# Kernel optimization log

Measured on AMD Instinct MI355X. Metric: run time of the kernel, lower is better.

The kernel has to match this reference:

```python
import jax, jax.numpy as jnp
import numpy as np

EPS = 1e-6

def setup_inputs() -> dict:
    key = jax.random.key(0)
    k1, k2 = jax.random.split(key)
    S, B, H, F = 2048, 4, 2048, 8192
    x = jax.random.normal(k1, (S, B, H), dtype=jnp.float32)
    scale = jnp.ones((H,), dtype=jnp.float32)
    ln_bias = jnp.zeros((H,), dtype=jnp.float32)
    kernel = jax.random.normal(k2, (H, F), dtype=jnp.float32) * 0.02  # ~variance_scaling fan_in
    return {"x": x, "scale": scale, "ln_bias": ln_bias, "kernel": kernel}

def reference(x, scale, ln_bias, kernel):
    # LayerNorm over last (hidden) axis, stats in fp32
    mu = jnp.mean(x, axis=-1, keepdims=True)
    var = jnp.mean(jnp.square(x - mu), axis=-1, keepdims=True)
    y = (x - mu) * jax.lax.rsqrt(var + EPS) * scale + ln_bias  # [S,B,H]
    # Dense: contract hidden axis against kernel [H,F]
    z = jnp.einsum('sbh,hf->sbf', y, kernel)  # [S,B,F]
    # return_layernorm_output=True -> (dense_out, ln_out)
    return (z, y)
```

## Files before the change

kernel.cpp:

```cpp
#include <hip/hip_runtime.h>
#include <stdint.h>


typedef __attribute__((ext_vector_type(8))) short short8;
typedef __attribute__((ext_vector_type(4))) float floatx4;

__device__ __forceinline__ unsigned short f2bf(float f) {
    unsigned u = __builtin_bit_cast(unsigned, f);
    u += 0x7fffu + ((u >> 16) & 1u);
    return (unsigned short)(u >> 16);
}

__global__ __launch_bounds__(256) void ln_kernel(
    const float* __restrict__ x, const float* __restrict__ scale,
    const float* __restrict__ bias, float* __restrict__ y,
    unsigned short* __restrict__ ybf, int H)
{
    const int row = blockIdx.x;
    const float* xr = x + (size_t)row * H;
    const int tid = threadIdx.x;

    float4 v0 = ((const float4*)xr)[tid];
    float4 v1 = ((const float4*)xr)[tid + 256];

    float s  = v0.x + v0.y + v0.z + v0.w + v1.x + v1.y + v1.z + v1.w;
    float ss = v0.x*v0.x + v0.y*v0.y + v0.z*v0.z + v0.w*v0.w
             + v1.x*v1.x + v1.y*v1.y + v1.z*v1.z + v1.w*v1.w;

    #pragma unroll
    for (int off = 32; off > 0; off >>= 1) {
        s  += __shfl_down(s,  off, 64);
        ss += __shfl_down(ss, off, 64);
    }
    __shared__ float rs[4], rq[4];
    if ((tid & 63) == 0) { rs[tid >> 6] = s; rq[tid >> 6] = ss; }
    __syncthreads();
    float ts = rs[0] + rs[1] + rs[2] + rs[3];
    float tq = rq[0] + rq[1] + rq[2] + rq[3];
    float mean = ts / (float)H;
    float var  = tq / (float)H - mean * mean;
    float rstd = rsqrtf(var + 1e-6f);

    float4 sc0 = ((const float4*)scale)[tid];
    float4 sc1 = ((const float4*)scale)[tid + 256];
    float4 b0  = ((const float4*)bias)[tid];
    float4 b1  = ((const float4*)bias)[tid + 256];

    float4 o0, o1;
    o0.x = (v0.x - mean) * rstd * sc0.x + b0.x;
    o0.y = (v0.y - mean) * rstd * sc0.y + b0.y;
    o0.z = (v0.z - mean) * rstd * sc0.z + b0.z;
    o0.w = (v0.w - mean) * rstd * sc0.w + b0.w;
    o1.x = (v1.x - mean) * rstd * sc1.x + b1.x;
    o1.y = (v1.y - mean) * rstd * sc1.y + b1.y;
    o1.z = (v1.z - mean) * rstd * sc1.z + b1.z;
    o1.w = (v1.w - mean) * rstd * sc1.w + b1.w;

    float* yr = y + (size_t)row * H;
    ((float4*)yr)[tid]       = o0;
    ((float4*)yr)[tid + 256] = o1;

    unsigned short* br = ybf + (size_t)row * H;
    uint2 p0, p1;
    p0.x = (unsigned)f2bf(o0.x) | ((unsigned)f2bf(o0.y) << 16);
    p0.y = (unsigned)f2bf(o0.z) | ((unsigned)f2bf(o0.w) << 16);
    p1.x = (unsigned)f2bf(o1.x) | ((unsigned)f2bf(o1.y) << 16);
    p1.y = (unsigned)f2bf(o1.z) | ((unsigned)f2bf(o1.w) << 16);
    ((uint2*)br)[tid]       = p0;
    ((uint2*)br)[tid + 256] = p1;
}

__global__ __launch_bounds__(256) void transpose_cast_kernel(
    const float* __restrict__ W, unsigned short* __restrict__ Bt,
    int K, int F)
{
    __shared__ float tile[64][65];
    const int kBase = blockIdx.y * 64;
    const int fBase = blockIdx.x * 64;
    const int tid = threadIdx.x;

    #pragma unroll
    for (int p = 0; p < 4; ++p) {
        int kl = (tid >> 4) + p * 16;
        int fl = (tid & 15) * 4;
        float4 v = *(const float4*)&W[(size_t)(kBase + kl) * F + fBase + fl];
        tile[kl][fl]     = v.x;
        tile[kl][fl + 1] = v.y;
        tile[kl][fl + 2] = v.z;
        tile[kl][fl + 3] = v.w;
    }
    __syncthreads();

    #pragma unroll
    for (int p = 0; p < 2; ++p) {
        int fl = (tid >> 3) + p * 32;
        int k8 = (tid & 7) * 8;
        unsigned w[4];
        #pragma unroll
        for (int j = 0; j < 4; ++j) {
            unsigned lo = f2bf(tile[k8 + 2*j][fl]);
            unsigned hi = f2bf(tile[k8 + 2*j + 1][fl]);
            w[j] = lo | (hi << 16);
        }
        uint4 out = make_uint4(w[0], w[1], w[2], w[3]);
        *(uint4*)&Bt[(size_t)(fBase + fl) * K + kBase + k8] = out;
    }
}

#define GBM 256
#define GBN 256
#define GBK 64

__device__ __forceinline__ void gload16(const unsigned short* src,
                                        unsigned short* dst) {
    __builtin_amdgcn_global_load_lds(
        (const __attribute__((address_space(1))) unsigned int*)src,
        (__attribute__((address_space(3))) unsigned int*)dst, 16, 0, 0);
}

__device__ __forceinline__ void stage_tile(
    const unsigned short* __restrict__ gA,
    const unsigned short* __restrict__ gB,
    unsigned short* dst, int t, int K, int o0, int d0)
{
    const int kb = t * GBK;
    #pragma unroll
    for (int j = 0; j < 4; ++j)
        gload16(gA + (size_t)(o0 + j * 64 * K + kb), dst + j * 4096 + d0);
    #pragma unroll
    for (int j = 0; j < 4; ++j)
        gload16(gB + (size_t)(o0 + j * 64 * K + kb), dst + 16384 + j * 4096 + d0);
}

template<int MH, int NH, bool LA, bool LB>
__device__ __forceinline__ void quad_phase(
    const unsigned short* bufA, const unsigned short* bufB,
    int rowA, int rowB, int s0, int s1,
    short8 (&a)[4][2], short8 (&b)[2][2], floatx4 (&acc)[8][4])
{
    if (LA) {
        #pragma unroll
        for (int i = 0; i < 4; ++i) {
            const unsigned short* rp = bufA + (MH * 64 + i * 16) * 64 + rowA;
            a[i][0] = *(const short8*)(rp + s0);
            a[i][1] = *(const short8*)(rp + s1);
        }
    }
    if (LB) {
        #pragma unroll
        for (int j = 0; j < 2; ++j) {
            const unsigned short* rp = bufB + ((NH * 2 + j) * 16) * 64 + rowB;
            b[j][0] = *(const short8*)(rp + s0);
            b[j][1] = *(const short8*)(rp + s1);
        }
    }
    __builtin_amdgcn_s_barrier();
    __builtin_amdgcn_s_setprio(1);
    #pragma unroll
    for (int i = 0; i < 4; ++i)
        #pragma unroll
        for (int j = 0; j < 2; ++j) {
            acc[MH*4+i][NH*2+j] = __builtin_amdgcn_mfma_f32_16x16x32_bf16(
                a[i][0], b[j][0], acc[MH*4+i][NH*2+j], 0, 0, 0);
            acc[MH*4+i][NH*2+j] = __builtin_amdgcn_mfma_f32_16x16x32_bf16(
                a[i][1], b[j][1], acc[MH*4+i][NH*2+j], 0, 0, 0);
        }
    __builtin_amdgcn_s_setprio(0);
    __builtin_amdgcn_s_barrier();
}

__global__ __launch_bounds__(512, 2) void gemm_bf16_8w(
    const unsigned short* __restrict__ A,
    const unsigned short* __restrict__ Bt,
    float* __restrict__ C,
    int M, int N, int K)
{
    __shared__ __align__(128) unsigned short lds[2][32768];

    const int tid   = threadIdx.x;
    const int lane  = tid & 63;
    const int wave  = tid >> 6;
    const int waveM = wave >> 2;
    const int waveN = wave & 3;
    const int quad  = lane >> 4;
    const int l16   = lane & 15;
    const int xs    = l16 & 7;
    const int s0    = (quad ^ xs) * 8;
    const int s1    = ((4 | quad) ^ xs) * 8;
    const int rowA  = l16 * 64;
    const int rowB  = ((waveN & 1) * 64 + l16) * 64;

    const int r0 = tid >> 3;
    const int g0 = (tid & 7) ^ (r0 & 7);
    const int o0 = r0 * K + g0 * 8;
    const int d0 = tid * 8;

    const int nwg = gridDim.x;
    const int cpx = nwg >> 3;
    const int bid = blockIdx.x;
    const int wg  = (bid & 7) * cpx + (bid >> 3);
    const int tilesN = N >> 8;
    const int tm = wg / tilesN;
    const int tn = wg % tilesN;

    const unsigned short* gA = A  + (size_t)tm * GBM * K;
    const unsigned short* gB = Bt + (size_t)tn * GBN * K;

    const int NT = K >> 6;

    floatx4 acc[8][4] = {};
    short8 a[4][2], b[2][2];

    unsigned short* bufA0 = &lds[0][0] + waveM * 8192;
    unsigned short* bufB0 = &lds[0][0] + 16384 + (waveN >> 1) * 8192;

    stage_tile(gA, gB, &lds[0][0], 0, K, o0, d0);
    stage_tile(gA, gB, &lds[1][0], 1, K, o0, d0);
    asm volatile("s_waitcnt vmcnt(8)" ::: "memory");
    __builtin_amdgcn_s_barrier();

    for (int t = 0; t < NT; t += 2) {
        quad_phase<0,0,true ,true >(bufA0, bufB0, rowA, rowB, s0, s1, a, b, acc);
        quad_phase<0,1,false,true >(bufA0, bufB0, rowA, rowB, s0, s1, a, b, acc);
        quad_phase<1,1,true ,false>(bufA0, bufB0, rowA, rowB, s0, s1, a, b, acc);
        quad_phase<1,0,false,true >(bufA0, bufB0, rowA, rowB, s0, s1, a, b, acc);
        {
            int ts = (t + 2 < NT) ? (t + 2) : (NT - 1);
            stage_tile(gA, gB, &lds[0][0], ts, K, o0, d0);
            asm volatile("s_waitcnt vmcnt(8)" ::: "memory");
            __builtin_amdgcn_s_barrier();
        }
        quad_phase<0,0,true ,true >(bufA0 + 32768, bufB0 + 32768, rowA, rowB, s0, s1, a, b, acc);
        quad_phase<0,1,false,true >(bufA0 + 32768, bufB0 + 32768, rowA, rowB, s0, s1, a, b, acc);
        quad_phase<1,1,true ,false>(bufA0 + 32768, bufB0 + 32768, rowA, rowB, s0, s1, a, b, acc);
        quad_phase<1,0,false,true >(bufA0 + 32768, bufB0 + 32768, rowA, rowB, s0, s1, a, b, acc);
        {
            int ts = (t + 3 < NT) ? (t + 3) : (NT - 1);
            stage_tile(gA, gB, &lds[1][0], ts, K, o0, d0);
            asm volatile("s_waitcnt vmcnt(8)" ::: "memory");
            __builtin_amdgcn_s_barrier();
        }
    }

    const size_t bm = (size_t)tm * GBM;
    const size_t bn = (size_t)tn * GBN;
    #pragma unroll
    for (int mi = 0; mi < 8; ++mi) {
        #pragma unroll
        for (int ni = 0; ni < 4; ++ni) {
            size_t col = bn + (size_t)waveN * 64 + ni * 16 + l16;
            #pragma unroll
            for (int r = 0; r < 4; ++r) {
                size_t row = bm + (size_t)waveM * 128 + mi * 16 + quad * 4 + r;
                C[row * N + col] = acc[mi][ni][r];
            }
        }
    }
}

extern "C" void kernel_launch(void* const* d_in, const int* in_sizes, int n_in,
                              void* d_out, int out_size, void* d_ws, size_t ws_size,
                              hipStream_t stream) {
    const float* x      = (const float*)d_in[0];
    const float* scale  = (const float*)d_in[1];
    const float* lnbias = (const float*)d_in[2];
    const float* W      = (const float*)d_in[3];

    const int H = in_sizes[1];
    const int M = in_sizes[0] / H;
    const int F = in_sizes[3] / H;

    float* z = (float*)d_out;
    float* y = z + (size_t)M * F;

    unsigned short* Abf = (unsigned short*)d_ws;
    unsigned short* Btb = Abf + (size_t)M * H;

    ln_kernel<<<M, 256, 0, stream>>>(x, scale, lnbias, y, Abf, H);
    transpose_cast_kernel<<<dim3(F / 64, H / 64), 256, 0, stream>>>(W, Btb, H, F);
    gemm_bf16_8w<<<dim3((M / GBM) * (F / GBN)), 512, 0, stream>>>(Abf, Btb, z, M, F, H);
}
```

Baseline: 705.6 us.

## Switch GEMM mainloop to 4-stage BK=32 pipeline with interleaved prefetch

Restructures the bf16 GEMM main loop from a double-buffered BK=64 scheme into a four-stage ring of BK=32 tiles, prefetching three tiles ahead. Each A and B tile load is issued between the LDS fragment reads and the MFMA block, and a new XOR swizzle is used for 32-wide rows. The aim is deeper latency hiding for global-to-LDS loads and fewer LDS reads per MFMA batch. The cost is twice as many barriers per unit of K, and the hand-tuned vmcnt accounting may not match the new load count.

```diff
diff --git a/kernel.cpp b/kernel.cpp
--- a/kernel.cpp
+++ b/kernel.cpp
@@ -109,7 +109,7 @@
 
 #define GBM 256
 #define GBN 256
-#define GBK 64
+#define GBK 32
 
 __device__ __forceinline__ void gload16(const unsigned short* src,
                                         unsigned short* dst) {
@@ -118,55 +118,17 @@
         (__attribute__((address_space(3))) unsigned int*)dst, 16, 0, 0);
 }
 
-__device__ __forceinline__ void stage_tile(
-    const unsigned short* __restrict__ gA,
-    const unsigned short* __restrict__ gB,
-    unsigned short* dst, int t, int K, int o0, int d0)
-{
-    const int kb = t * GBK;
-    #pragma unroll
-    for (int j = 0; j < 4; ++j)
-        gload16(gA + (size_t)(o0 + j * 64 * K + kb), dst + j * 4096 + d0);
-    #pragma unroll
-    for (int j = 0; j < 4; ++j)
-        gload16(gB + (size_t)(o0 + j * 64 * K + kb), dst + 16384 + j * 4096 + d0);
-}
-
-template<int MH, int NH, bool LA, bool LB>
-__device__ __forceinline__ void quad_phase(
-    const unsigned short* bufA, const unsigned short* bufB,
-    int rowA, int rowB, int s0, int s1,
-    short8 (&a)[4][2], short8 (&b)[2][2], floatx4 (&acc)[8][4])
-{
-    if (LA) {
-        #pragma unroll
-        for (int i = 0; i < 4; ++i) {
-            const unsigned short* rp = bufA + (MH * 64 + i * 16) * 64 + rowA;
-            a[i][0] = *(const short8*)(rp + s0);
-            a[i][1] = *(const short8*)(rp + s1);
-        }
-    }
-    if (LB) {
-        #pragma unroll
-        for (int j = 0; j < 2; ++j) {
-            const unsigned short* rp = bufB + ((NH * 2 + j) * 16) * 64 + rowB;
-            b[j][0] = *(const short8*)(rp + s0);
-            b[j][1] = *(const short8*)(rp + s1);
-        }
-    }
-    __builtin_amdgcn_s_barrier();
-    __builtin_amdgcn_s_setprio(1);
-    #pragma unroll
-    for (int i = 0; i < 4; ++i)
-        #pragma unroll
-        for (int j = 0; j < 2; ++j) {
-            acc[MH*4+i][NH*2+j] = __builtin_amdgcn_mfma_f32_16x16x32_bf16(
-                a[i][0], b[j][0], acc[MH*4+i][NH*2+j], 0, 0, 0);
-            acc[MH*4+i][NH*2+j] = __builtin_amdgcn_mfma_f32_16x16x32_bf16(
-                a[i][1], b[j][1], acc[MH*4+i][NH*2+j], 0, 0, 0);
-        }
-    __builtin_amdgcn_s_setprio(0);
-    __builtin_amdgcn_s_barrier();
+__device__ __forceinline__ void stage_op(
+    const unsigned short* __restrict__ g, unsigned short* dst,
+    int t, int K, int tid)
+{
+    #pragma unroll
+    for (int i = 0; i < 2; ++i) {
+        int e = i * 512 + tid;
+        int r = e >> 2;
+        int c = (e & 3) ^ ((r >> 1) & 3);
+        gload16(g + (size_t)r * K + t * GBK + c * 8, dst + e * 8);
+    }
 }
 
 __global__ __launch_bounds__(512, 2) void gemm_bf16_8w(
@@ -175,7 +137,7 @@
     float* __restrict__ C,
     int M, int N, int K)
 {
-    __shared__ __align__(128) unsigned short lds[2][32768];
+    __shared__ __align__(128) unsigned short lds[4][16384];
 
     const int tid   = threadIdx.x;
     const int lane  = tid & 63;
@@ -184,16 +146,9 @@
     const int waveN = wave & 3;
     const int quad  = lane >> 4;
     const int l16   = lane & 15;
-    const int xs    = l16 & 7;
-    const int s0    = (quad ^ xs) * 8;
-    const int s1    = ((4 | quad) ^ xs) * 8;
-    const int rowA  = l16 * 64;
-    const int rowB  = ((waveN & 1) * 64 + l16) * 64;
-
-    const int r0 = tid >> 3;
-    const int g0 = (tid & 7) ^ (r0 & 7);
-    const int o0 = r0 * K + g0 * 8;
-    const int d0 = tid * 8;
+    const int soff  = (quad ^ ((l16 >> 1) & 3)) * 8;
+    const int rowA0 = waveM * 128 + l16;
+    const int rowB0 = waveN * 64 + l16;
 
     const int nwg = gridDim.x;
     const int cpx = nwg >> 3;
@@ -206,37 +161,66 @@
     const unsigned short* gA = A  + (size_t)tm * GBM * K;
     const unsigned short* gB = Bt + (size_t)tn * GBN * K;
 
-    const int NT = K >> 6;
+    const int NT = K >> 5;
 
     floatx4 acc[8][4] = {};
-    short8 a[4][2], b[2][2];
-
-    unsigned short* bufA0 = &lds[0][0] + waveM * 8192;
-    unsigned short* bufB0 = &lds[0][0] + 16384 + (waveN >> 1) * 8192;
-
-    stage_tile(gA, gB, &lds[0][0], 0, K, o0, d0);
-    stage_tile(gA, gB, &lds[1][0], 1, K, o0, d0);
+
+    stage_op(gA, &lds[0][0],    0, K, tid);
+    stage_op(gB, &lds[0][8192], 0, K, tid);
+    stage_op(gA, &lds[1][0],    1, K, tid);
+    stage_op(gB, &lds[1][8192], 1, K, tid);
+    stage_op(gA, &lds[2][0],    2, K, tid);
+    stage_op(gB, &lds[2][8192], 2, K, tid);
     asm volatile("s_waitcnt vmcnt(8)" ::: "memory");
     __builtin_amdgcn_s_barrier();
 
-    for (int t = 0; t < NT; t += 2) {
-        quad_phase<0,0,true ,true >(bufA0, bufB0, rowA, rowB, s0, s1, a, b, acc);
-        quad_phase<0,1,false,true >(bufA0, bufB0, rowA, rowB, s0, s1, a, b, acc);
-        quad_phase<1,1,true ,false>(bufA0, bufB0, rowA, rowB, s0, s1, a, b, acc);
-        quad_phase<1,0,false,true >(bufA0, bufB0, rowA, rowB, s0, s1, a, b, acc);
-        {
-            int ts = (t + 2 < NT) ? (t + 2) : (NT - 1);
-            stage_tile(gA, gB, &lds[0][0], ts, K, o0, d0);
-            asm volatile("s_waitcnt vmcnt(8)" ::: "memory");
-            __builtin_amdgcn_s_barrier();
-        }
-        quad_phase<0,0,true ,true >(bufA0 + 32768, bufB0 + 32768, rowA, rowB, s0, s1, a, b, acc);
-        quad_phase<0,1,false,true >(bufA0 + 32768, bufB0 + 32768, rowA, rowB, s0, s1, a, b, acc);
-        quad_phase<1,1,true ,false>(bufA0 + 32768, bufB0 + 32768, rowA, rowB, s0, s1, a, b, acc);
-        quad_phase<1,0,false,true >(bufA0 + 32768, bufB0 + 32768, rowA, rowB, s0, s1, a, b, acc);
-        {
-            int ts = (t + 3 < NT) ? (t + 3) : (NT - 1);
-            stage_tile(gA, gB, &lds[1][0], ts, K, o0, d0);
+    for (int t = 0; t < NT; t += 4) {
+        #pragma unroll
+        for (int u = 0; u < 4; ++u) {
+            const int tt = t + u;
+            const unsigned short* bufA = &lds[u][0];
+            const unsigned short* bufB = &lds[u][8192];
+            unsigned short* pre = &lds[(u + 3) & 3][0];
+            int ts = tt + 3; if (ts > NT - 1) ts = NT - 1;
+
+            short8 a[4], b[4];
+            #pragma unroll
+            for (int i = 0; i < 4; ++i)
+                a[i] = *(const short8*)(bufA + (rowA0 + i * 16) * 32 + soff);
+            #pragma unroll
+            for (int j = 0; j < 4; ++j)
+                b[j] = *(const short8*)(bufB + (rowB0 + j * 16) * 32 + soff);
+            stage_op(gA, pre, ts, K, tid);
+            __builtin_amdgcn_sched_barrier(0);
+            __builtin_amdgcn_s_barrier();
+            asm volatile("s_waitcnt lgkmcnt(0)" ::: "memory");
+            __builtin_amdgcn_sched_barrier(0);
+            __builtin_amdgcn_s_setprio(1);
+            #pragma unroll
+            for (int i = 0; i < 4; ++i)
+                #pragma unroll
+                for (int j = 0; j < 4; ++j)
+                    acc[i][j] = __builtin_amdgcn_mfma_f32_16x16x32_bf16(
+                        a[i], b[j], acc[i][j], 0, 0, 0);
+            __builtin_amdgcn_s_setprio(0);
+            __builtin_amdgcn_s_barrier();
+
+            #pragma unroll
+            for (int i = 0; i < 4; ++i)
+                a[i] = *(const short8*)(bufA + (rowA0 + 64 + i * 16) * 32 + soff);
+            stage_op(gB, pre + 8192, ts, K, tid);
+            __builtin_amdgcn_sched_barrier(0);
+            __builtin_amdgcn_s_barrier();
+            asm volatile("s_waitcnt lgkmcnt(0)" ::: "memory");
+            __builtin_amdgcn_sched_barrier(0);
+            __builtin_amdgcn_s_setprio(1);
+            #pragma unroll
+            for (int i = 0; i < 4; ++i)
+                #pragma unroll
+                for (int j = 0; j < 4; ++j)
+                    acc[4 + i][j] = __builtin_amdgcn_mfma_f32_16x16x32_bf16(
+                        a[i], b[j], acc[4 + i][j], 0, 0, 0);
+            __builtin_amdgcn_s_setprio(0);
             asm volatile("s_waitcnt vmcnt(8)" ::: "memory");
             __builtin_amdgcn_s_barrier();
         }
```

Measured after the change: 689.7 us. 2.2% less time.
